# Kernel optimization log

Measured on AMD Instinct MI355X. Metric: run time of the kernel, lower is better.

## Reference

```python
import jax, jax.numpy as jnp
import numpy as np

B, N, C = 4, 2048, 768
H = 12
D = C // H  # head_dim = 64
SCALE = D ** -0.5


def setup_inputs() -> dict:
    key = jax.random.key(0)
    ks = jax.random.split(key, 9)
    x_q = jax.random.normal(ks[0], (B, N, C), dtype=jnp.float32)
    x_k = jax.random.normal(ks[1], (B, N, C), dtype=jnp.float32)
    x_v = jax.random.normal(ks[2], (B, N, C), dtype=jnp.float32)
    x_u = jax.random.uniform(ks[3], (B, N, C), dtype=jnp.float32)
    s = C ** -0.5
    Wq = jax.random.normal(ks[4], (C, C), dtype=jnp.float32) * s
    Wk = jax.random.normal(ks[5], (C, C), dtype=jnp.float32) * s
    Wv = jax.random.normal(ks[6], (C, C), dtype=jnp.float32) * s
    Wp = jax.random.normal(ks[7], (C, C), dtype=jnp.float32) * s
    bp = jax.random.normal(ks[8], (C,), dtype=jnp.float32) * 0.01
    return {"x_q": x_q, "x_k": x_k, "x_v": x_v, "x_u": x_u,
            "Wq": Wq, "Wk": Wk, "Wv": Wv, "Wp": Wp, "bp": bp}


def reference(x_q, x_k, x_v, x_u, Wq, Wk, Wv, Wp, bp):
    # Linear projections (torch Linear: y = x @ W.T), split into heads [B,H,N,D]
    def to_heads(x, W):
        y = jnp.einsum('bnc,oc->bno', x, W)
        return y.reshape(B, N, H, D).transpose(0, 2, 1, 3)
    q = to_heads(x_q, Wq) * SCALE
    k = to_heads(x_k, Wk)
    v = to_heads(x_v, Wv)
    # Scores [B,H,N,N]
    attn = jnp.einsum('bhqd,bhkd->bhqk', q, k)
    # Uncertainty map: per-query scalar (mean over channels), broadcast over keys & heads
    uc = jnp.mean(x_u, axis=-1)  # [B,N]
    attn = attn * uc[:, None, :, None]
    attn = jax.nn.softmax(attn, axis=-1)
    out = jnp.einsum('bhqk,bhkd->bhqd', attn, v)
    out = out.transpose(0, 2, 1, 3).reshape(B, N, C)
    return jnp.einsum('bnc,oc->bno', out, Wp) + bp
```

## Files before the change

### kernel.cpp

```cpp
#include <hip/hip_runtime.h>
#include <hip/hip_bf16.h>
#include <cstdint>

#define B_ 4
#define N_ 2048
#define C_ 768
#define H_ 12
#define D_ 64
#define QSCALE 0.18033688011112042f

typedef __bf16 bf16x8 __attribute__((ext_vector_type(8)));
typedef float f32x4 __attribute__((ext_vector_type(4)));

__device__ __forceinline__ unsigned f2bs(float x) {
  unsigned u = __builtin_bit_cast(unsigned, x);
  unsigned r = (u + 0x7fffu + ((u >> 16) & 1u)) >> 16;
  return r;
}

__device__ __forceinline__ bf16x8 ldb8(const unsigned short* p) {
  return __builtin_bit_cast(bf16x8, *(const uint4*)p);
}

__device__ __forceinline__ f32x4 mfma16(bf16x8 a, bf16x8 b, f32x4 c) {
  return __builtin_amdgcn_mfma_f32_16x16x32_bf16(a, b, c, 0, 0, 0);
}

__device__ __forceinline__ void async16(const unsigned short* g, unsigned short* l) {
  __builtin_amdgcn_global_load_lds(
      (const __attribute__((address_space(1))) unsigned int*)g,
      (__attribute__((address_space(3))) unsigned int*)l, 16, 0, 0);
}

__global__ void prep_kernel(
    const float* __restrict__ xq, const float* __restrict__ xk,
    const float* __restrict__ xv, const float* __restrict__ xu,
    const float* __restrict__ Wq, const float* __restrict__ Wk,
    const float* __restrict__ Wv, const float* __restrict__ Wp,
    unsigned short* __restrict__ dxq, unsigned short* __restrict__ dxk,
    unsigned short* __restrict__ dxv,
    unsigned short* __restrict__ dwq, unsigned short* __restrict__ dwk,
    unsigned short* __restrict__ dwv, unsigned short* __restrict__ dwp,
    float* __restrict__ uc) {
  const int id = blockIdx.x;
  if (id < 18432) {
    const float* s = (id < 6144) ? xq : (id < 12288) ? xk : xv;
    unsigned short* d = (id < 6144) ? dxq : (id < 12288) ? dxk : dxv;
    int i = ((id % 6144) * 256 + threadIdx.x) * 4;
    float4 v = *(const float4*)(s + i);
    ushort4 h;
    h.x = (unsigned short)f2bs(v.x); h.y = (unsigned short)f2bs(v.y);
    h.z = (unsigned short)f2bs(v.z); h.w = (unsigned short)f2bs(v.w);
    *(ushort4*)(d + i) = h;
  } else if (id < 20736) {
    int sub = id - 18432;
    int which = sub / 576;
    const float* s = (which == 0) ? Wq : (which == 1) ? Wk : (which == 2) ? Wv : Wp;
    unsigned short* d = (which == 0) ? dwq : (which == 1) ? dwk : (which == 2) ? dwv : dwp;
    int i = ((sub % 576) * 256 + threadIdx.x) * 4;
    float4 v = *(const float4*)(s + i);
    ushort4 h;
    h.x = (unsigned short)f2bs(v.x); h.y = (unsigned short)f2bs(v.y);
    h.z = (unsigned short)f2bs(v.z); h.w = (unsigned short)f2bs(v.w);
    *(ushort4*)(d + i) = h;
  } else {
    int sub = id - 20736;
    int w = threadIdx.x >> 6, lane = threadIdx.x & 63;
    int row = sub * 4 + w;
    const float* p = xu + (size_t)row * C_;
    float s = 0.f;
#pragma unroll
    for (int i = 0; i < 3; ++i) {
      float4 v = *(const float4*)(p + (i * 64 + lane) * 4);
      s += v.x + v.y + v.z + v.w;
    }
#pragma unroll
    for (int off = 1; off < 64; off <<= 1) s += __shfl_xor(s, off);
    if (lane == 0) uc[row] = s * (1.f / 768.f);
  }
}

__device__ __forceinline__ void gemm_mainloop(
    const unsigned short* __restrict__ A, const unsigned short* __restrict__ W,
    int m0, int n0, unsigned short* Al, unsigned short* Bl,
    int tid, int wm, int wn, int quad, int id15, f32x4 (*acc)[4]) {
  const int wb = tid & 192;
  const unsigned short* ap[4];
  const unsigned short* bp[4];
#pragma unroll
  for (int s = 0; s < 4; ++s) {
    int g = s * 256 + tid;
    int row = (g >> 2) & 127;
    int col = ((g >> 9) << 5) | ((g & 3) << 3);
    ap[s] = A + (size_t)(m0 + row) * C_ + col;
    bp[s] = W + (size_t)(n0 + row) * C_ + col;
  }

  for (int kt = 0; kt < C_; kt += 64) {
    __syncthreads();
#pragma unroll
    for (int s = 0; s < 4; ++s) {
      async16(ap[s] + kt, Al + (s * 256 + wb) * 8);
      async16(bp[s] + kt, Bl + (s * 256 + wb) * 8);
    }
    __syncthreads();

#pragma unroll
    for (int kk = 0; kk < 2; ++kk) {
      bf16x8 af[4], bfr[4];
#pragma unroll
      for (int i = 0; i < 4; ++i)
        af[i]  = ldb8(&Al[kk * 4096 + (wm + i * 16 + id15) * 32 + quad * 8]);
#pragma unroll
      for (int j = 0; j < 4; ++j)
        bfr[j] = ldb8(&Bl[kk * 4096 + (wn + j * 16 + id15) * 32 + quad * 8]);
#pragma unroll
      for (int i = 0; i < 4; ++i)
#pragma unroll
        for (int j = 0; j < 4; ++j)
          acc[i][j] = mfma16(af[i], bfr[j], acc[i][j]);
    }
  }
}

#define TSTR 136
__global__ __launch_bounds__(256, 3) void gemm_qkv(
    const unsigned short* __restrict__ xq, const unsigned short* __restrict__ xk,
    const unsigned short* __restrict__ xv,
    const unsigned short* __restrict__ wq, const unsigned short* __restrict__ wk,
    const unsigned short* __restrict__ wv,
    unsigned short* __restrict__ oq, unsigned short* __restrict__ ok,
    unsigned short* __restrict__ ov, const float* __restrict__ uc) {
  __shared__ __align__(16) unsigned short S[128 * TSTR];
  unsigned short* Al = S;
  unsigned short* Bl = S + 8192;
  const int tid = threadIdx.x;
  const int w = tid >> 6, lane = tid & 63, quad = lane >> 4, id15 = lane & 15;
  const int wm = (w >> 1) << 6, wn = (w & 1) << 6;
  const int id = blockIdx.x;
  const int xcd = id & 7, slot = id >> 3;
  const int n0 = (slot % 6) << 7;
  const int gz = xcd * 24 + slot / 6;
  const int z = gz >> 6, m0 = (gz & 63) << 7;

  const unsigned short* A = (z == 0) ? xq : (z == 1) ? xk : xv;
  const unsigned short* W = (z == 0) ? wq : (z == 1) ? wk : wv;

  f32x4 acc[4][4] = {};
  gemm_mainloop(A, W, m0, n0, Al, Bl, tid, wm, wn, quad, id15, acc);

  if (z == 2) {
    __syncthreads();
#pragma unroll
    for (int i = 0; i < 4; ++i)
#pragma unroll
      for (int j = 0; j < 4; ++j) {
        uint2 u;
        u.x = f2bs(acc[i][j][0]) | (f2bs(acc[i][j][1]) << 16);
        u.y = f2bs(acc[i][j][2]) | (f2bs(acc[i][j][3]) << 16);
        *(uint2*)&S[(wn + j * 16 + id15) * TSTR + wm + i * 16 + quad * 4] = u;
      }
    __syncthreads();
    const int b = m0 >> 11, nb = m0 & (N_ - 1);
#pragma unroll
    for (int s = 0; s < 8; ++s) {
      int c = s * 256 + tid;
      int row = c >> 4, o = (c & 15) << 3;
      *(uint4*)(ov + (size_t)(b * C_ + n0 + row) * N_ + nb + o) = *(const uint4*)&S[row * TSTR + o];
    }
    return;
  }

#pragma unroll
  for (int i = 0; i < 4; ++i) {
#pragma unroll
    for (int j = 0; j < 4; ++j) {
#pragma unroll
      for (int r = 0; r < 4; ++r) {
        int gm = m0 + wm + i * 16 + quad * 4 + r;
        int gn = n0 + wn + j * 16 + id15;
        float v = acc[i][j][r];
        if (z == 0) {
          v *= QSCALE * uc[gm];
          oq[(size_t)gm * C_ + gn] = (unsigned short)f2bs(v);
        } else {
          ok[(size_t)gm * C_ + gn] = (unsigned short)f2bs(v);
        }
      }
    }
  }
}

__global__ __launch_bounds__(256, 4) void gemm_out(
    const unsigned short* __restrict__ ao, const unsigned short* __restrict__ wp,
    float* __restrict__ out, const float* __restrict__ bias) {
  __shared__ __align__(16) unsigned short Al[64 * 64];
  __shared__ __align__(16) unsigned short Bl[128 * 64];
  const int tid = threadIdx.x;
  const int w = tid >> 6, lane = tid & 63, quad = lane >> 4, id15 = lane & 15;
  const int wm = (w >> 1) << 5, wn = (w & 1) << 6;
  const int id = blockIdx.x;
  const int xcd = id & 7, slot = id >> 3;
  const int n0 = (slot % 6) << 7;
  const int m0 = (xcd * 16 + slot / 6) << 6;

  const int wb = tid & 192;
  const unsigned short* ap[2];
#pragma unroll
  for (int s = 0; s < 2; ++s) {
    int g = s * 256 + tid;
    int row = (g >> 2) & 63;
    int col = ((g >> 8) << 5) | ((g & 3) << 3);
    ap[s] = ao + (size_t)(m0 + row) * C_ + col;
  }
  const unsigned short* bp[4];
#pragma unroll
  for (int s = 0; s < 4; ++s) {
    int g = s * 256 + tid;
    int row = (g >> 2) & 127;
    int col = ((g >> 9) << 5) | ((g & 3) << 3);
    bp[s] = wp + (size_t)(n0 + row) * C_ + col;
  }

  f32x4 acc[2][4] = {};
  for (int kt = 0; kt < C_; kt += 64) {
    __syncthreads();
#pragma unroll
    for (int s = 0; s < 2; ++s) async16(ap[s] + kt, Al + (s * 256 + wb) * 8);
#pragma unroll
    for (int s = 0; s < 4; ++s) async16(bp[s] + kt, Bl + (s * 256 + wb) * 8);
    __syncthreads();

#pragma unroll
    for (int kk = 0; kk < 2; ++kk) {
      bf16x8 af[2], bfr[4];
#pragma unroll
      for (int i = 0; i < 2; ++i)
        af[i]  = ldb8(&Al[kk * 2048 + (wm + i * 16 + id15) * 32 + quad * 8]);
#pragma unroll
      for (int j = 0; j < 4; ++j)
        bfr[j] = ldb8(&Bl[kk * 4096 + (wn + j * 16 + id15) * 32 + quad * 8]);
#pragma unroll
      for (int i = 0; i < 2; ++i)
#pragma unroll
        for (int j = 0; j < 4; ++j)
          acc[i][j] = mfma16(af[i], bfr[j], acc[i][j]);
    }
  }

#pragma unroll
  for (int i = 0; i < 2; ++i) {
#pragma unroll
    for (int j = 0; j < 4; ++j) {
#pragma unroll
      for (int r = 0; r < 4; ++r) {
        int gm = m0 + wm + i * 16 + quad * 4 + r;
        int gn = n0 + wn + j * 16 + id15;
        out[(size_t)gm * C_ + gn] = acc[i][j][r] + bias[gn];
      }
    }
  }
}

#define KSTR 72
#define PSTR 72
__global__ __launch_bounds__(256, 3) void attn_kernel(
    const unsigned short* __restrict__ Q, const unsigned short* __restrict__ Kk,
    const unsigned short* __restrict__ Vt, unsigned short* __restrict__ O) {
  __shared__ __align__(16) unsigned short Kl[64 * KSTR];
  __shared__ __align__(16) unsigned short Vl[64 * KSTR];
  __shared__ __align__(16) unsigned short Pl[8][16 * PSTR];

  const int tid = threadIdx.x;
  const int w = tid >> 6, lane = tid & 63, quad = lane >> 4, id15 = lane & 15;
  const int id = blockIdx.x;
  const int xcd = id & 7, slot = id >> 3;
  const int bh = xcd * 6 + (slot >> 4);
  const int qt = slot & 15;
  const int b = bh / H_, h = bh % H_;
  const int q0 = qt * 128 + w * 32;

  bf16x8 qf[2][2];
#pragma unroll
  for (int rg = 0; rg < 2; ++rg)
#pragma unroll
    for (int kb = 0; kb < 2; ++kb)
      qf[rg][kb] = ldb8(Q + (size_t)(b * N_ + q0 + rg * 16 + id15) * C_ + h * 64 + kb * 32 + quad * 8);

  const uint4 onesu = {0x3F803F80u, 0x3F803F80u, 0x3F803F80u, 0x3F803F80u};
  const bf16x8 onesf = __builtin_bit_cast(bf16x8, onesu);

  f32x4 oacc[2][4] = {};
  f32x4 lacc[2] = {};

  const size_t kbase = (size_t)(b * N_) * C_ + h * 64;
  const size_t vbase = (size_t)(b * C_ + h * 64) * N_;
  const int srow0 = tid >> 3, srow1 = (256 + tid) >> 3;
  const int sseg0 = (tid & 7) << 3;

  unsigned short* Plw0 = &Pl[w * 2 + 0][0];
  unsigned short* Plw1 = &Pl[w * 2 + 1][0];

  for (int kc = 0; kc < N_; kc += 64) {
    __syncthreads();
    *(uint4*)&Kl[srow0 * KSTR + sseg0] = *(const uint4*)(Kk + kbase + (size_t)(kc + srow0) * C_ + sseg0);
    *(uint4*)&Kl[srow1 * KSTR + sseg0] = *(const uint4*)(Kk + kbase + (size_t)(kc + srow1) * C_ + sseg0);
    *(uint4*)&Vl[srow0 * KSTR + sseg0] = *(const uint4*)(Vt + vbase + (size_t)srow0 * N_ + kc + sseg0);
    *(uint4*)&Vl[srow1 * KSTR + sseg0] = *(const uint4*)(Vt + vbase + (size_t)srow1 * N_ + kc + sseg0);
    __syncthreads();

    f32x4 sA[4], sB[4];
#pragma unroll
    for (int cb = 0; cb < 4; ++cb) {
      f32x4 a = {}, c = {};
#pragma unroll
      for (int kb = 0; kb < 2; ++kb) {
        bf16x8 kf = ldb8(&Kl[(cb * 16 + id15) * KSTR + kb * 32 + quad * 8]);
        a = mfma16(kf, qf[0][kb], a);
        c = mfma16(kf, qf[1][kb], c);
      }
      sA[cb] = a; sB[cb] = c;
    }

#pragma unroll
    for (int rg = 0; rg < 2; ++rg) {
      f32x4* s4 = (rg == 0) ? sA : sB;
      unsigned short* Plw = (rg == 0) ? Plw0 : Plw1;
#pragma unroll
      for (int cb = 0; cb < 4; ++cb) {
        unsigned p0 = __builtin_bit_cast(unsigned, exp2f(s4[cb][0]));
        unsigned p1 = __builtin_bit_cast(unsigned, exp2f(s4[cb][1]));
        unsigned p2 = __builtin_bit_cast(unsigned, exp2f(s4[cb][2]));
        unsigned p3 = __builtin_bit_cast(unsigned, exp2f(s4[cb][3]));
        uint2 u;
        u.x = __builtin_amdgcn_perm(p1, p0, 0x07060302u);
        u.y = __builtin_amdgcn_perm(p3, p2, 0x07060302u);
        *(uint2*)&Plw[id15 * PSTR + cb * 16 + quad * 4] = u;
      }
    }

    bf16x8 pf[2][2];
#pragma unroll
    for (int kb = 0; kb < 2; ++kb) {
      pf[0][kb] = ldb8(&Plw0[id15 * PSTR + kb * 32 + quad * 8]);
      pf[1][kb] = ldb8(&Plw1[id15 * PSTR + kb * 32 + quad * 8]);
    }

#pragma unroll
    for (int kb = 0; kb < 2; ++kb) {
      lacc[0] = mfma16(pf[0][kb], onesf, lacc[0]);
      lacc[1] = mfma16(pf[1][kb], onesf, lacc[1]);
    }
#pragma unroll
    for (int db = 0; db < 4; ++db) {
#pragma unroll
      for (int kb = 0; kb < 2; ++kb) {
        bf16x8 vf = ldb8(&Vl[(db * 16 + id15) * KSTR + kb * 32 + quad * 8]);
        oacc[0][db] = mfma16(pf[0][kb], vf, oacc[0][db]);
        oacc[1][db] = mfma16(pf[1][kb], vf, oacc[1][db]);
      }
    }
  }

#pragma unroll
  for (int rg = 0; rg < 2; ++rg) {
#pragma unroll
    for (int r = 0; r < 4; ++r) {
      float linv = 1.0f / lacc[rg][r];
      int n = q0 + rg * 16 + quad * 4 + r;
#pragma unroll
      for (int db = 0; db < 4; ++db)
        O[(size_t)(b * N_ + n) * C_ + h * 64 + db * 16 + id15] = (unsigned short)f2bs(oacc[rg][db][r] * linv);
    }
  }
}

extern "C" void kernel_launch(void* const* d_in, const int* in_sizes, int n_in,
                              void* d_out, int out_size, void* d_ws, size_t ws_size,
                              hipStream_t stream) {
  const float* x_q = (const float*)d_in[0];
  const float* x_k = (const float*)d_in[1];
  const float* x_v = (const float*)d_in[2];
  const float* x_u = (const float*)d_in[3];
  const float* Wq  = (const float*)d_in[4];
  const float* Wk  = (const float*)d_in[5];
  const float* Wv  = (const float*)d_in[6];
  const float* Wp  = (const float*)d_in[7];
  const float* bp  = (const float*)d_in[8];

  char* ws = (char*)d_ws;
  size_t off = 0;
  auto alloc = [&](size_t bytes) {
    char* p = ws + off;
    off += (bytes + 255) & ~(size_t)255;
    return p;
  };
  unsigned short* wq16 = (unsigned short*)alloc((size_t)C_ * C_ * 2);
  unsigned short* wk16 = (unsigned short*)alloc((size_t)C_ * C_ * 2);
  unsigned short* wv16 = (unsigned short*)alloc((size_t)C_ * C_ * 2);
  unsigned short* wp16 = (unsigned short*)alloc((size_t)C_ * C_ * 2);
  float*          ucp  = (float*)alloc((size_t)B_ * N_ * 4);
  unsigned short* xq16 = (unsigned short*)alloc((size_t)B_ * N_ * C_ * 2);
  unsigned short* xk16 = (unsigned short*)alloc((size_t)B_ * N_ * C_ * 2);
  unsigned short* xv16 = (unsigned short*)alloc((size_t)B_ * N_ * C_ * 2);
  unsigned short* q_s  = (unsigned short*)alloc((size_t)B_ * N_ * C_ * 2);
  unsigned short* k_s  = (unsigned short*)alloc((size_t)B_ * N_ * C_ * 2);
  unsigned short* vT   = (unsigned short*)alloc((size_t)B_ * N_ * C_ * 2);
  unsigned short* ao   = (unsigned short*)alloc((size_t)B_ * N_ * C_ * 2);

  prep_kernel<<<dim3(22784), 256, 0, stream>>>(x_q, x_k, x_v, x_u, Wq, Wk, Wv, Wp,
                                               xq16, xk16, xv16,
                                               wq16, wk16, wv16, wp16, ucp);
  gemm_qkv<<<dim3(1152), 256, 0, stream>>>(xq16, xk16, xv16, wq16, wk16, wv16,
                                           q_s, k_s, vT, ucp);
  attn_kernel<<<dim3(768), 256, 0, stream>>>(q_s, k_s, vT, ao);
  gemm_out<<<dim3(768), 256, 0, stream>>>(ao, wp16, (float*)d_out, bp);
}
```

Measured before the change: 296.4 us.

## Double-buffer async global-to-LDS loads with XOR swizzle in GEMMs and attention

Converts the QKV GEMM, output GEMM and attention mainloops to a two-stage pipeline. The next tiles are prefetched into LDS with global_load_lds while the current tile is computed, and explicit vmcnt waits and barriers replace the double __syncthreads. The LDS layout is XOR-swizzled so the padded strides can be dropped without bank conflicts, and attention switches from synchronous register copies to async loads. The larger LDS footprint lowers the occupancy bounds. The prologue and tail issue redundant wrapped-around loads.

```diff
diff --git a/kernel.cpp b/kernel.cpp
--- a/kernel.cpp
+++ b/kernel.cpp
@@ -9,13 +9,17 @@
 #define D_ 64
 #define QSCALE 0.18033688011112042f
 
+#define WAIT_VM0 0x0F70
+#define WAIT_VM4 0x0F74
+#define WAIT_VM6 0x0F76
+#define WAIT_VM8 0x0F78
+
 typedef __bf16 bf16x8 __attribute__((ext_vector_type(8)));
 typedef float f32x4 __attribute__((ext_vector_type(4)));
 
 __device__ __forceinline__ unsigned f2bs(float x) {
   unsigned u = __builtin_bit_cast(unsigned, x);
-  unsigned r = (u + 0x7fffu + ((u >> 16) & 1u)) >> 16;
-  return r;
+  return (u + 0x7fffu + ((u >> 16) & 1u)) >> 16;
 }
 
 __device__ __forceinline__ bf16x8 ldb8(const unsigned short* p) {
@@ -80,60 +84,80 @@
   }
 }
 
-__device__ __forceinline__ void gemm_mainloop(
+__device__ __forceinline__ void gemm_mainloop_db(
     const unsigned short* __restrict__ A, const unsigned short* __restrict__ W,
-    int m0, int n0, unsigned short* Al, unsigned short* Bl,
+    int m0, int n0, unsigned short* Ab, unsigned short* Bb,
     int tid, int wm, int wn, int quad, int id15, f32x4 (*acc)[4]) {
   const int wb = tid & 192;
   const unsigned short* ap[4];
   const unsigned short* bp[4];
+  int dst[4];
 #pragma unroll
   for (int s = 0; s < 4; ++s) {
     int g = s * 256 + tid;
-    int row = (g >> 2) & 127;
-    int col = ((g >> 9) << 5) | ((g & 3) << 3);
-    ap[s] = A + (size_t)(m0 + row) * C_ + col;
-    bp[s] = W + (size_t)(n0 + row) * C_ + col;
-  }
-
-  for (int kt = 0; kt < C_; kt += 64) {
-    __syncthreads();
-#pragma unroll
-    for (int s = 0; s < 4; ++s) {
-      async16(ap[s] + kt, Al + (s * 256 + wb) * 8);
-      async16(bp[s] + kt, Bl + (s * 256 + wb) * 8);
-    }
-    __syncthreads();
-
+    int row = g >> 3;
+    int gs = (g & 7) ^ (row & 7);
+    ap[s] = A + (size_t)(m0 + row) * C_ + gs * 8;
+    bp[s] = W + (size_t)(n0 + row) * C_ + gs * 8;
+    dst[s] = (s * 256 + wb) * 8;
+  }
+  auto issue = [&](int p, int si) {
+    int kt = (si >= 12 ? si - 12 : si) * 64;
+#pragma unroll
+    for (int s = 0; s < 4; ++s) async16(ap[s] + kt, Ab + p * 8192 + dst[s]);
+#pragma unroll
+    for (int s = 0; s < 4; ++s) async16(bp[s] + kt, Bb + p * 8192 + dst[s]);
+  };
+  issue(0, 0);
+  issue(1, 1);
+  const int sw0 = (quad ^ (id15 & 7)) * 8;
+  const int sw1 = ((4 + quad) ^ (id15 & 7)) * 8;
+
+  for (int si = 0; si < 12; ++si) {
+    const int p = si & 1;
+    __builtin_amdgcn_sched_barrier(0);
+    __builtin_amdgcn_s_waitcnt(WAIT_VM8);
+    __builtin_amdgcn_s_barrier();
+    __builtin_amdgcn_sched_barrier(0);
+
+    const unsigned short* Ap = Ab + p * 8192;
+    const unsigned short* Bp = Bb + p * 8192;
 #pragma unroll
     for (int kk = 0; kk < 2; ++kk) {
+      const int sw = kk ? sw1 : sw0;
       bf16x8 af[4], bfr[4];
 #pragma unroll
       for (int i = 0; i < 4; ++i)
-        af[i]  = ldb8(&Al[kk * 4096 + (wm + i * 16 + id15) * 32 + quad * 8]);
+        af[i]  = ldb8(Ap + (wm + i * 16 + id15) * 64 + sw);
 #pragma unroll
       for (int j = 0; j < 4; ++j)
-        bfr[j] = ldb8(&Bl[kk * 4096 + (wn + j * 16 + id15) * 32 + quad * 8]);
+        bfr[j] = ldb8(Bp + (wn + j * 16 + id15) * 64 + sw);
 #pragma unroll
       for (int i = 0; i < 4; ++i)
 #pragma unroll
         for (int j = 0; j < 4; ++j)
           acc[i][j] = mfma16(af[i], bfr[j], acc[i][j]);
     }
-  }
+
+    __builtin_amdgcn_sched_barrier(0);
+    __builtin_amdgcn_s_barrier();
+    __builtin_amdgcn_sched_barrier(0);
+    issue(p, si + 2);
+  }
+  __builtin_amdgcn_s_waitcnt(WAIT_VM0);
 }
 
 #define TSTR 136
-__global__ __launch_bounds__(256, 3) void gemm_qkv(
+__global__ __launch_bounds__(256, 2) void gemm_qkv(
     const unsigned short* __restrict__ xq, const unsigned short* __restrict__ xk,
     const unsigned short* __restrict__ xv,
     const unsigned short* __restrict__ wq, const unsigned short* __restrict__ wk,
     const unsigned short* __restrict__ wv,
     unsigned short* __restrict__ oq, unsigned short* __restrict__ ok,
     unsigned short* __restrict__ ov, const float* __restrict__ uc) {
-  __shared__ __align__(16) unsigned short S[128 * TSTR];
-  unsigned short* Al = S;
-  unsigned short* Bl = S + 8192;
+  __shared__ __align__(16) unsigned short Lds[32768];
+  unsigned short* Ab = Lds;
+  unsigned short* Bb = Lds + 16384;
   const int tid = threadIdx.x;
   const int w = tid >> 6, lane = tid & 63, quad = lane >> 4, id15 = lane & 15;
   const int wm = (w >> 1) << 6, wn = (w & 1) << 6;
@@ -147,10 +171,11 @@
   const unsigned short* W = (z == 0) ? wq : (z == 1) ? wk : wv;
 
   f32x4 acc[4][4] = {};
-  gemm_mainloop(A, W, m0, n0, Al, Bl, tid, wm, wn, quad, id15, acc);
+  gemm_mainloop_db(A, W, m0, n0, Ab, Bb, tid, wm, wn, quad, id15, acc);
 
   if (z == 2) {
     __syncthreads();
+    unsigned short* S = Lds;
 #pragma unroll
     for (int i = 0; i < 4; ++i)
 #pragma unroll
@@ -191,11 +216,11 @@
   }
 }
 
-__global__ __launch_bounds__(256, 4) void gemm_out(
+__global__ __launch_bounds__(256, 3) void gemm_out(
     const unsigned short* __restrict__ ao, const unsigned short* __restrict__ wp,
     float* __restrict__ out, const float* __restrict__ bias) {
-  __shared__ __align__(16) unsigned short Al[64 * 64];
-  __shared__ __align__(16) unsigned short Bl[128 * 64];
+  __shared__ __align__(16) unsigned short Ab[2 * 4096];
+  __shared__ __align__(16) unsigned short Bb[2 * 8192];
   const int tid = threadIdx.x;
   const int w = tid >> 6, lane = tid & 63, quad = lane >> 4, id15 = lane & 15;
   const int wm = (w >> 1) << 5, wn = (w & 1) << 6;
@@ -206,47 +231,70 @@
 
   const int wb = tid & 192;
   const unsigned short* ap[2];
+  int adst[2];
 #pragma unroll
   for (int s = 0; s < 2; ++s) {
     int g = s * 256 + tid;
-    int row = (g >> 2) & 63;
-    int col = ((g >> 8) << 5) | ((g & 3) << 3);
-    ap[s] = ao + (size_t)(m0 + row) * C_ + col;
+    int row = g >> 3;
+    int gs = (g & 7) ^ (row & 7);
+    ap[s] = ao + (size_t)(m0 + row) * C_ + gs * 8;
+    adst[s] = (s * 256 + wb) * 8;
   }
   const unsigned short* bp[4];
+  int bdst[4];
 #pragma unroll
   for (int s = 0; s < 4; ++s) {
     int g = s * 256 + tid;
-    int row = (g >> 2) & 127;
-    int col = ((g >> 9) << 5) | ((g & 3) << 3);
-    bp[s] = wp + (size_t)(n0 + row) * C_ + col;
-  }
+    int row = g >> 3;
+    int gs = (g & 7) ^ (row & 7);
+    bp[s] = wp + (size_t)(n0 + row) * C_ + gs * 8;
+    bdst[s] = (s * 256 + wb) * 8;
+  }
+  auto issue = [&](int p, int si) {
+    int kt = (si >= 12 ? si - 12 : si) * 64;
+#pragma unroll
+    for (int s = 0; s < 2; ++s) async16(ap[s] + kt, Ab + p * 4096 + adst[s]);
+#pragma unroll
+    for (int s = 0; s < 4; ++s) async16(bp[s] + kt, Bb + p * 8192 + bdst[s]);
+  };
+  issue(0, 0);
+  issue(1, 1);
+  const int sw0 = (quad ^ (id15 & 7)) * 8;
+  const int sw1 = ((4 + quad) ^ (id15 & 7)) * 8;
 
   f32x4 acc[2][4] = {};
-  for (int kt = 0; kt < C_; kt += 64) {
-    __syncthreads();
-#pragma unroll
-    for (int s = 0; s < 2; ++s) async16(ap[s] + kt, Al + (s * 256 + wb) * 8);
-#pragma unroll
-    for (int s = 0; s < 4; ++s) async16(bp[s] + kt, Bl + (s * 256 + wb) * 8);
-    __syncthreads();
-
+  for (int si = 0; si < 12; ++si) {
+    const int p = si & 1;
+    __builtin_amdgcn_sched_barrier(0);
+    __builtin_amdgcn_s_waitcnt(WAIT_VM6);
+    __builtin_amdgcn_s_barrier();
+    __builtin_amdgcn_sched_barrier(0);
+
+    const unsigned short* Ap = Ab + p * 4096;
+    const unsigned short* Bp = Bb + p * 8192;
 #pragma unroll
     for (int kk = 0; kk < 2; ++kk) {
+      const int sw = kk ? sw1 : sw0;
       bf16x8 af[2], bfr[4];
 #pragma unroll
       for (int i = 0; i < 2; ++i)
-        af[i]  = ldb8(&Al[kk * 2048 + (wm + i * 16 + id15) * 32 + quad * 8]);
+        af[i]  = ldb8(Ap + (wm + i * 16 + id15) * 64 + sw);
 #pragma unroll
       for (int j = 0; j < 4; ++j)
-        bfr[j] = ldb8(&Bl[kk * 4096 + (wn + j * 16 + id15) * 32 + quad * 8]);
+        bfr[j] = ldb8(Bp + (wn + j * 16 + id15) * 64 + sw);
 #pragma unroll
       for (int i = 0; i < 2; ++i)
 #pragma unroll
         for (int j = 0; j < 4; ++j)
           acc[i][j] = mfma16(af[i], bfr[j], acc[i][j]);
     }
-  }
+
+    __builtin_amdgcn_sched_barrier(0);
+    __builtin_amdgcn_s_barrier();
+    __builtin_amdgcn_sched_barrier(0);
+    issue(p, si + 2);
+  }
+  __builtin_amdgcn_s_waitcnt(WAIT_VM0);
 
 #pragma unroll
   for (int i = 0; i < 2; ++i) {
@@ -262,13 +310,12 @@
   }
 }
 
-#define KSTR 72
 #define PSTR 72
 __global__ __launch_bounds__(256, 3) void attn_kernel(
     const unsigned short* __restrict__ Q, const unsigned short* __restrict__ Kk,
     const unsigned short* __restrict__ Vt, unsigned short* __restrict__ O) {
-  __shared__ __align__(16) unsigned short Kl[64 * KSTR];
-  __shared__ __align__(16) unsigned short Vl[64 * KSTR];
+  __shared__ __align__(16) unsigned short Kb[2][4096];
+  __shared__ __align__(16) unsigned short Vb[2][4096];
   __shared__ __align__(16) unsigned short Pl[8][16 * PSTR];
 
   const int tid = threadIdx.x;
@@ -295,30 +342,57 @@
 
   const size_t kbase = (size_t)(b * N_) * C_ + h * 64;
   const size_t vbase = (size_t)(b * C_ + h * 64) * N_;
-  const int srow0 = tid >> 3, srow1 = (256 + tid) >> 3;
-  const int sseg0 = (tid & 7) << 3;
+
+  const int wb = tid & 192;
+  const unsigned short* kp[2];
+  const unsigned short* vp[2];
+  int dstq[2];
+#pragma unroll
+  for (int s = 0; s < 2; ++s) {
+    int g = s * 256 + tid;
+    int row = g >> 3;
+    int gs = (g & 7) ^ (row & 7);
+    kp[s] = Kk + kbase + (size_t)row * C_ + gs * 8;
+    vp[s] = Vt + vbase + (size_t)row * N_ + gs * 8;
+    dstq[s] = (s * 256 + wb) * 8;
+  }
+  auto issue = [&](int p, int ci) {
+    int kc = (ci & 31) * 64;
+    async16(kp[0] + (size_t)kc * C_, &Kb[p][dstq[0]]);
+    async16(kp[1] + (size_t)kc * C_, &Kb[p][dstq[1]]);
+    async16(vp[0] + kc, &Vb[p][dstq[0]]);
+    async16(vp[1] + kc, &Vb[p][dstq[1]]);
+  };
+  issue(0, 0);
+  issue(1, 1);
+  const int sw0 = (quad ^ (id15 & 7)) * 8;
+  const int sw1 = ((4 + quad) ^ (id15 & 7)) * 8;
+  const int r64 = id15 * 64;
 
   unsigned short* Plw0 = &Pl[w * 2 + 0][0];
   unsigned short* Plw1 = &Pl[w * 2 + 1][0];
 
-  for (int kc = 0; kc < N_; kc += 64) {
-    __syncthreads();
-    *(uint4*)&Kl[srow0 * KSTR + sseg0] = *(const uint4*)(Kk + kbase + (size_t)(kc + srow0) * C_ + sseg0);
-    *(uint4*)&Kl[srow1 * KSTR + sseg0] = *(const uint4*)(Kk + kbase + (size_t)(kc + srow1) * C_ + sseg0);
-    *(uint4*)&Vl[srow0 * KSTR + sseg0] = *(const uint4*)(Vt + vbase + (size_t)srow0 * N_ + kc + sseg0);
-    *(uint4*)&Vl[srow1 * KSTR + sseg0] = *(const uint4*)(Vt + vbase + (size_t)srow1 * N_ + kc + sseg0);
-    __syncthreads();
+  for (int ci = 0; ci < 32; ++ci) {
+    const int p = ci & 1;
+    __builtin_amdgcn_sched_barrier(0);
+    __builtin_amdgcn_s_waitcnt(WAIT_VM4);
+    __builtin_amdgcn_s_barrier();
+    __builtin_amdgcn_sched_barrier(0);
+
+    const unsigned short* Kp = &Kb[p][0];
+    const unsigned short* Vp = &Vb[p][0];
 
     f32x4 sA[4], sB[4];
 #pragma unroll
     for (int cb = 0; cb < 4; ++cb) {
       f32x4 a = {}, c = {};
-#pragma unroll
-      for (int kb = 0; kb < 2; ++kb) {
-        bf16x8 kf = ldb8(&Kl[(cb * 16 + id15) * KSTR + kb * 32 + quad * 8]);
-        a = mfma16(kf, qf[0][kb], a);
-        c = mfma16(kf, qf[1][kb], c);
-      }
+      const unsigned short* kr = Kp + cb * 1024 + r64;
+      bf16x8 kf0 = ldb8(kr + sw0);
+      a = mfma16(kf0, qf[0][0], a);
+      c = mfma16(kf0, qf[1][0], c);
+      bf16x8 kf1 = ldb8(kr + sw1);
+      a = mfma16(kf1, qf[0][1], a);
+      c = mfma16(kf1, qf[1][1], c);
       sA[cb] = a; sB[cb] = c;
     }
 
@@ -353,14 +427,21 @@
     }
 #pragma unroll
     for (int db = 0; db < 4; ++db) {
-#pragma unroll
-      for (int kb = 0; kb < 2; ++kb) {
-        bf16x8 vf = ldb8(&Vl[(db * 16 + id15) * KSTR + kb * 32 + quad * 8]);
-        oacc[0][db] = mfma16(pf[0][kb], vf, oacc[0][db]);
-        oacc[1][db] = mfma16(pf[1][kb], vf, oacc[1][db]);
-      }
-    }
-  }
+      const unsigned short* vr = Vp + db * 1024 + r64;
+      bf16x8 vf0 = ldb8(vr + sw0);
+      oacc[0][db] = mfma16(pf[0][0], vf0, oacc[0][db]);
+      oacc[1][db] = mfma16(pf[1][0], vf0, oacc[1][db]);
+      bf16x8 vf1 = ldb8(vr + sw1);
+      oacc[0][db] = mfma16(pf[0][1], vf1, oacc[0][db]);
+      oacc[1][db] = mfma16(pf[1][1], vf1, oacc[1][db]);
+    }
+
+    __builtin_amdgcn_sched_barrier(0);
+    __builtin_amdgcn_s_barrier();
+    __builtin_amdgcn_sched_barrier(0);
+    issue(p, ci + 2);
+  }
+  __builtin_amdgcn_s_waitcnt(WAIT_VM0);
 
 #pragma unroll
   for (int rg = 0; rg < 2; ++rg) {
```

Result: slower. 309.9 us (+4.5%).
